# Optimization experiments

Measured on AMD Instinct MI355X. Metric: run time of the kernel, lower is better.

Reference implementation:

```python
import jax, jax.numpy as jnp
import numpy as np

IMAGE_SIZE = 288.0
LAMBDA_NOOBJ = 0.5
LAMBDA_COOR = 5.0
_ANCHOR_DIMS = np.array([[0.24, 0.24], [0.12, 0.12], [0.08, 0.08], [0.28, 0.28], [0.15, 0.15]], np.float32)
ANCHORS = jnp.concatenate([jnp.full((5, 2), 0.5, jnp.float32), jnp.asarray(_ANCHOR_DIMS)], axis=1)  # [cx,cy,w,h]


def _corners(box):
    # matches torch _format_bbox column order used in _get_iou: (x1, x2, y1, y2)
    cx, cy, w, h = box[..., 0], box[..., 1], box[..., 2], box[..., 3]
    return cx - w / 2, cx + w / 2, cy - h / 2, cy + h / 2


def _iou(b1, b2):
    x1a, x2a, y1a, y2a = _corners(b1)
    x1b, x2b, y1b, y2b = _corners(b2)
    iw = jnp.minimum(x2a, x2b) - jnp.maximum(x1a, x1b) + 1.0
    ih = jnp.minimum(y2a, y2b) - jnp.maximum(y1a, y1b) + 1.0
    inter = iw * ih
    a1 = (x2a - x1a + 1.0) * (y2a - y1a + 1.0)
    a2 = (x2b - x1b + 1.0) * (y2b - y1b + 1.0)
    return inter / (a1 + a2 - inter + 1e-16)


def setup_inputs() -> dict:
    key = jax.random.key(0)
    k1, k2, k3, k4 = jax.random.split(key, 4)
    B, G, A, T = 32, 36, 5, 8
    return {
        "bbox_prediction": jax.random.normal(k1, (B, G, G, A, 5), jnp.float32),
        "landmarks_prediction": jax.random.normal(k2, (B, G, G, A, 68, 2), jnp.float32),
        "bbox_target": jax.random.uniform(k3, (B, T, 4), jnp.float32),
        "landmarks_target": jax.random.uniform(k4, (B, T, 68, 2), jnp.float32),
    }


def _forward(bbox_prediction, landmarks_prediction, bbox_target, landmarks_target):
    B, G, _, A, _ = bbox_prediction.shape
    T = bbox_target.shape[1]
    N = B * G * G * A

    valid = bbox_target.sum(-1) != 0  # (B,T)
    gx = bbox_target[..., 0] * G
    gy = bbox_target[..., 1] * G
    gi = jnp.floor(gx).astype(jnp.int32)  # int(gt_x)
    gj = jnp.floor(gy).astype(jnp.int32)
    fx = gx - gi
    fy = gy - gj
    gt_anchor_box = jnp.stack([fx, fy, bbox_target[..., 2], bbox_target[..., 3]], -1)  # (B,T,4)

    # vectorized anchor assignment (replaces per-target python loop)
    anchor_iou = _iou(gt_anchor_box[:, :, None, :], ANCHORS[None, None, :, :])  # (B,T,A)
    best_a = jnp.argmax(anchor_iou, -1).astype(jnp.int32)
    log_box = jnp.log1p(gt_anchor_box)  # (B,T,4) -- torch stores log1p form

    lin = ((jnp.arange(B)[:, None] * G + gj) * G + gi) * A + best_a  # (B,T) flat (b,j,i,a)
    lin = jnp.where(valid, lin, N)  # invalid targets -> dump slot N

    obj = jnp.zeros(N + 1, jnp.float32).at[lin.ravel()].set(1.0)[:N].reshape(B, G, G, A)
    noobj = 1.0 - obj

    t_ids = jnp.broadcast_to(jnp.arange(T, dtype=jnp.int32), (B, T))
    seg_last = jax.ops.segment_max(t_ids.ravel(), lin.ravel(), num_segments=N + 1)
    winner = (seg_last[lin] == t_ids) & valid
    lin_w = jnp.where(winner, lin, N).ravel()

    gt_boxes = jnp.zeros((N + 1, 4), jnp.float32).at[lin_w].set(log_box.reshape(-1, 4))[:N].reshape(B, G, G, A, 4)
    gt_lm = jnp.zeros((N + 1, 136), jnp.float32).at[lin_w].set(landmarks_target.reshape(B * T, 136))[:N].reshape(B, G, G, A, 136)

    nobj = jnp.maximum(obj.sum(), 1.0)

    # NME over object cells (masked-mean expressed as weighted sum -> static shapes)
    diff = landmarks_prediction.reshape(B, G, G, A, 136) - gt_lm
    dist = jnp.sqrt(jnp.sum(diff * diff, -1))  # (B,G,G,A)
    wh = gt_boxes[..., 2] * gt_boxes[..., 3]  # note: log1p(w)*log1p(h), as in torch
    norm = jnp.sqrt(jnp.where(obj > 0, wh, 1.0)) * IMAGE_SIZE * 68.0 * nobj
    nme = jnp.sum(obj * dist / norm)

    # localization: SmoothL1 (beta=1), mean over masked elements
    d = bbox_prediction[..., :4] - gt_boxes
    ad = jnp.abs(d)
    sl1 = jnp.where(ad < 1.0, 0.5 * d * d, ad - 0.5)
    loc_loss = LAMBDA_COOR * jnp.sum(obj[..., None] * sl1) / (nobj * 4.0)

    # confidence: MSE on noobj (target 0) + MSE on obj (target 1)
    conf_pred = bbox_prediction[..., 4]
    n_noobj = jnp.maximum(noobj.sum(), 1.0)
    conf_loss = LAMBDA_NOOBJ * jnp.sum(noobj * conf_pred ** 2) / n_noobj + jnp.sum(obj * (conf_pred - 1.0) ** 2) / nobj

    # best predicted bbox per target (IoU of log1p gt box vs raw cell predictions, as in torch)
    cell_pred = bbox_prediction[jnp.arange(B)[:, None], gj, gi]  # (B,T,A,5)
    pred_iou = _iou(log_box[:, :, None, :], cell_pred[..., :4])  # (B,T,A)
    best_p = jnp.argmax(pred_iou, -1)
    best = jnp.take_along_axis(cell_pred, best_p[..., None, None], axis=2)[:, :, 0]  # (B,T,5)
    x1, x2, y1, y2 = _corners(best[..., :4])
    best_pred = jnp.where(valid[..., None], jnp.stack([x1, x2, y1, y2, best[..., 4]], -1), 0.0)

    return nme, loc_loss, conf_loss, best_pred


def reference(bbox_prediction, landmarks_prediction, bbox_target, landmarks_target):
    return _forward(bbox_prediction, landmarks_prediction, bbox_target, landmarks_target)
```

## Files before the change

### kernel.cpp

```cpp
#include <hip/hip_runtime.h>
#include <math.h>

#define Gc 36
#define Ac 5
#define Bc 32
#define Tc 8
#define NCELLS (Bc*Gc*Gc*Ac)
#define NFLOATS (NCELLS*5)
#define NF4 (NFLOATS/4)
#define NT 256
#define CONF_BLOCKS 128
#define GRID (CONF_BLOCKS + 256)


__device__ __forceinline__ void target_meta(const float* __restrict__ bbox_tgt,
                                            int tgt, bool& valid, int& gi, int& gj,
                                            float& fx, float& fy, float& w, float& h,
                                            int& best_a) {
    const float* tg = bbox_tgt + (size_t)tgt * 4;
    float x = tg[0], y = tg[1];
    w = tg[2]; h = tg[3];
    valid = ((x + y + w + h) != 0.0f);
    float gx = x * (float)Gc, gy = y * (float)Gc;
    gi = (int)floorf(gx); gj = (int)floorf(gy);
    fx = gx - floorf(gx); fy = gy - floorf(gy);

    float x1a = fx - w * 0.5f, x2a = fx + w * 0.5f;
    float y1a = fy - h * 0.5f, y2a = fy + h * 0.5f;
    float a1 = (x2a - x1a + 1.0f) * (y2a - y1a + 1.0f);
    const float adim[Ac] = {0.24f, 0.12f, 0.08f, 0.28f, 0.15f};
    best_a = 0;
    float best_iou = -1e30f;
    for (int a = 0; a < Ac; ++a) {
        float x1b = 0.5f - adim[a] * 0.5f, x2b = 0.5f + adim[a] * 0.5f;
        float iw = fminf(x2a, x2b) - fmaxf(x1a, x1b) + 1.0f;
        float ih = fminf(y2a, x2b) - fmaxf(y1a, x1b) + 1.0f;
        float inter = iw * ih;
        float a2 = (x2b - x1b + 1.0f) * (x2b - x1b + 1.0f);
        float iou = inter / (a1 + a2 - inter + 1e-16f);
        if (iou > best_iou) { best_iou = iou; best_a = a; }
    }
}

__device__ __forceinline__ void do_conf(const float* __restrict__ bbox_pred,
                                        float* __restrict__ ws_f) {
    __shared__ float red[NT];
    const float4* p4 = (const float4*)bbox_pred;
    float acc = 0.0f;
    for (int j = blockIdx.x * NT + threadIdx.x; j < NF4;
         j += CONF_BLOCKS * NT) {
        float4 f = p4[j];
        int r = (4 * j) % 5;
        float v = (r == 4) ? f.x : (r == 3) ? f.y : (r == 2) ? f.z
                : (r == 1) ? f.w : 0.0f;
        acc += v * v;
    }
    red[threadIdx.x] = acc;
    __syncthreads();
    for (int s = NT / 2; s > 0; s >>= 1) {
        if (threadIdx.x < s) red[threadIdx.x] += red[threadIdx.x + s];
        __syncthreads();
    }
    if (threadIdx.x == 0) ws_f[blockIdx.x] = red[0];
}

__device__ __forceinline__ void do_target(const float* __restrict__ lm_pred,
                                          const float* __restrict__ bbox_tgt,
                                          const float* __restrict__ lm_tgt,
                                          float* __restrict__ ws_f,
                                          int* __restrict__ ws_i) {
    const int tgt = blockIdx.x - CONF_BLOCKS;
    const int b = tgt >> 3, t = tgt & 7;
    const int tid = threadIdx.x;
    __shared__ int s_lin8[8];

    if (tid < 8) {
        bool v; int gi, gj, ba; float fx, fy, w, h;
        target_meta(bbox_tgt, (b << 3) + tid, v, gi, gj, fx, fy, w, h, ba);
        s_lin8[tid] = v ? (((b * Gc + gj) * Gc + gi) * Ac + ba) : NCELLS;
    }
    __syncthreads();

    if (tid < 64) {
        int lin = s_lin8[t];
        bool valid = (lin != NCELLS);
        bool winner = valid;
        if (valid)
            for (int t2 = t + 1; t2 < Tc; ++t2)
                if (s_lin8[t2] == lin) { winner = false; break; }

        float acc = 0.0f;
        if (winner && tid < 34) {
            const float4* lp = (const float4*)(lm_pred + (size_t)lin * 136);
            const float4* lt = (const float4*)(lm_tgt + (size_t)tgt * 136);
            float4 a = lp[tid], c = lt[tid];
            float dx = a.x - c.x, dy = a.y - c.y;
            float dz = a.z - c.z, dw = a.w - c.w;
            acc = dx * dx + dy * dy + dz * dz + dw * dw;
        }
        for (int off = 32; off > 0; off >>= 1)
            acc += __shfl_down(acc, off, 64);

        if (tid == 0) {
            ws_i[256 + tgt] = lin;
            ws_i[512 + tgt] = winner ? 1 : 0;
            ws_f[1024 + tgt] = winner ? sqrtf(acc) : 0.0f;
        }
    }
}

__device__ __forceinline__ void do_final(const float* __restrict__ bbox_pred,
                                         const float* __restrict__ bbox_tgt,
                                         const float* __restrict__ ws_f,
                                         const int* __restrict__ ws_i,
                                         float* __restrict__ out) {
    const int tid = threadIdx.x;
    const int b = tid >> 3;
    __shared__ float4 s_red4[NT];
    __shared__ float  s_reds[NT];
    __shared__ int    s_cnt[NT];

    bool valid; int gi, gj, best_a; float fx, fy, w, h;
    target_meta(bbox_tgt, tid, valid, gi, gj, fx, fy, w, h, best_a);
    int lin = ws_i[256 + tid];
    int winner = ws_i[512 + tid];
    float dist = ws_f[1024 + tid];

    float l0 = log1pf(fx), l1 = log1pf(fy), l2 = log1pf(w), l3 = log1pf(h);

    float c_nme = 0.0f, c_sl1 = 0.0f, c_cobj = 0.0f, c_csq = 0.0f;
    if (winner) {
        const float* bp = bbox_pred + (size_t)lin * 5;
        float conf = bp[4];
        c_cobj = (conf - 1.0f) * (conf - 1.0f);
        c_csq = conf * conf;
        float lb[4] = {l0, l1, l2, l3};
        for (int k = 0; k < 4; ++k) {
            float d = bp[k] - lb[k];
            float ad = fabsf(d);
            c_sl1 += (ad < 1.0f) ? 0.5f * d * d : (ad - 0.5f);
        }
        c_nme = dist / (sqrtf(l2 * l3) * 288.0f * 68.0f);
    }

    s_cnt[tid] = winner;
    s_red4[tid] = make_float4(c_nme, c_sl1, c_cobj, c_csq);
    s_reds[tid] = (tid < CONF_BLOCKS) ? ws_f[tid] : 0.0f;
    __syncthreads();
    for (int s = NT / 2; s > 0; s >>= 1) {
        if (tid < s) {
            s_cnt[tid] += s_cnt[tid + s];
            float4 a = s_red4[tid], c = s_red4[tid + s];
            a.x += c.x; a.y += c.y; a.z += c.z; a.w += c.w;
            s_red4[tid] = a;
            s_reds[tid] += s_reds[tid + s];
        }
        __syncthreads();
    }

    if (tid == 0) {
        int cnt = s_cnt[0];
        float nobj = fmaxf((float)cnt, 1.0f);
        float n_noobj = fmaxf((float)(NCELLS - cnt), 1.0f);
        float4 sums = s_red4[0];
        float s_total = s_reds[0];
        out[0] = sums.x / nobj;
        out[1] = 5.0f * sums.y / (nobj * 4.0f);
        out[2] = 0.5f * (s_total - sums.w) / n_noobj + sums.z / nobj;
    }

    const float* cp = bbox_pred + (size_t)((b * Gc + gj) * Gc + gi) * Ac * 5;
    float x1g = l0 - l2 * 0.5f, x2g = l0 + l2 * 0.5f;
    float y1g = l1 - l3 * 0.5f, y2g = l1 + l3 * 0.5f;
    float ag = (x2g - x1g + 1.0f) * (y2g - y1g + 1.0f);
    int bp_idx = 0;
    float bp_iou = -1e30f;
    for (int a = 0; a < Ac; ++a) {
        float cx = cp[a * 5 + 0], cy = cp[a * 5 + 1];
        float pw = cp[a * 5 + 2], ph = cp[a * 5 + 3];
        float x1p = cx - pw * 0.5f, x2p = cx + pw * 0.5f;
        float y1p = cy - ph * 0.5f, y2p = cy + ph * 0.5f;
        float iw = fminf(x2g, x2p) - fmaxf(x1g, x1p) + 1.0f;
        float ih = fminf(y2g, y2p) - fmaxf(y1g, y1p) + 1.0f;
        float inter = iw * ih;
        float ap = (x2p - x1p + 1.0f) * (y2p - y1p + 1.0f);
        float iou = inter / (ag + ap - inter + 1e-16f);
        if (iou > bp_iou) { bp_iou = iou; bp_idx = a; }
    }
    float bx = cp[bp_idx * 5 + 0], by = cp[bp_idx * 5 + 1];
    float bw = cp[bp_idx * 5 + 2], bh = cp[bp_idx * 5 + 3];
    float bconf = cp[bp_idx * 5 + 4];
    float* op = out + 3 + (size_t)tid * 5;
    if (valid) {
        op[0] = bx - bw * 0.5f; op[1] = bx + bw * 0.5f;
        op[2] = by - bh * 0.5f; op[3] = by + bh * 0.5f; op[4] = bconf;
    } else {
        op[0] = 0.0f; op[1] = 0.0f; op[2] = 0.0f; op[3] = 0.0f; op[4] = 0.0f;
    }
}

__global__ __launch_bounds__(NT) void k_all(
        const float* __restrict__ bbox_pred,
        const float* __restrict__ lm_pred,
        const float* __restrict__ bbox_tgt,
        const float* __restrict__ lm_tgt,
        float* ws_f, int* ws_i,
        float* __restrict__ out) {
    if (blockIdx.x < CONF_BLOCKS) {
        do_conf(bbox_pred, ws_f);
    } else {
        do_target(lm_pred, bbox_tgt, lm_tgt, ws_f, ws_i);
    }

    __shared__ int s_last;
    if (threadIdx.x == 0) {
        __threadfence();
        unsigned int old = atomicAdd((unsigned int*)(ws_i + 2048), 1u);
        int last = (old == (unsigned int)(GRID - 1));
        if (last) __threadfence();
        s_last = last;
    }
    __syncthreads();

    if (s_last) {
        do_final(bbox_pred, bbox_tgt, ws_f, ws_i, out);
    }
}

extern "C" void kernel_launch(void* const* d_in, const int* in_sizes, int n_in,
                              void* d_out, int out_size, void* d_ws, size_t ws_size,
                              hipStream_t stream) {
    const float* bbox_pred = (const float*)d_in[0];
    const float* lm_pred   = (const float*)d_in[1];
    const float* bbox_tgt  = (const float*)d_in[2];
    const float* lm_tgt    = (const float*)d_in[3];
    float* out = (float*)d_out;
    float* ws_f = (float*)d_ws;
    int* ws_i = (int*)d_ws;

    hipMemsetAsync((char*)d_ws + 2048 * sizeof(int), 0, sizeof(unsigned int),
                   stream);

    k_all<<<GRID, NT, 0, stream>>>(bbox_pred, lm_pred, bbox_tgt, lm_tgt,
                                   ws_f, ws_i, out);
}
```

Measured before the change: 162.9 us.

## Replace last-block atomic handoff with two kernel launches and move best-pred to target blocks

Splits the single fused kernel, which used an atomic counter with threadfences to pick the last block for the final reduction, into two launches: one for the confidence and landmark partials and one single-block final kernel. This drops the memset and the atomic/fence handshake. The best-predicted-box IoU search moves from the final block into the per-target blocks, so the final kernel's serial tail is shorter. In exchange there is an extra kernel launch boundary.

New measurement: 152.4 us. 6.4% less time.

```diff
diff --git a/kernel.cpp b/kernel.cpp
--- a/kernel.cpp
+++ b/kernel.cpp
@@ -10,7 +10,6 @@
 #define NF4 (NFLOATS/4)
 #define NT 256
 #define CONF_BLOCKS 128
-#define GRID (CONF_BLOCKS + 256)
 
 
 __device__ __forceinline__ void target_meta(const float* __restrict__ bbox_tgt,
@@ -42,80 +41,119 @@
     }
 }
 
-__device__ __forceinline__ void do_conf(const float* __restrict__ bbox_pred,
-                                        float* __restrict__ ws_f) {
-    __shared__ float red[NT];
-    const float4* p4 = (const float4*)bbox_pred;
-    float acc = 0.0f;
-    for (int j = blockIdx.x * NT + threadIdx.x; j < NF4;
-         j += CONF_BLOCKS * NT) {
-        float4 f = p4[j];
-        int r = (4 * j) % 5;
-        float v = (r == 4) ? f.x : (r == 3) ? f.y : (r == 2) ? f.z
-                : (r == 1) ? f.w : 0.0f;
-        acc += v * v;
-    }
-    red[threadIdx.x] = acc;
-    __syncthreads();
-    for (int s = NT / 2; s > 0; s >>= 1) {
-        if (threadIdx.x < s) red[threadIdx.x] += red[threadIdx.x + s];
+__global__ __launch_bounds__(NT) void k12_conf_lm(
+        const float* __restrict__ bbox_pred,
+        const float* __restrict__ lm_pred,
+        const float* __restrict__ bbox_tgt,
+        const float* __restrict__ lm_tgt,
+        float* __restrict__ ws_f, int* __restrict__ ws_i,
+        float* __restrict__ out) {
+    if (blockIdx.x < CONF_BLOCKS) {
+        __shared__ float red[NT];
+        const float4* p4 = (const float4*)bbox_pred;
+        float acc = 0.0f;
+        for (int j = blockIdx.x * NT + threadIdx.x; j < NF4;
+             j += CONF_BLOCKS * NT) {
+            float4 f = p4[j];
+            int r = (4 * j) % 5;
+            float v = (r == 4) ? f.x : (r == 3) ? f.y : (r == 2) ? f.z
+                    : (r == 1) ? f.w : 0.0f;
+            acc += v * v;
+        }
+        red[threadIdx.x] = acc;
         __syncthreads();
-    }
-    if (threadIdx.x == 0) ws_f[blockIdx.x] = red[0];
-}
-
-__device__ __forceinline__ void do_target(const float* __restrict__ lm_pred,
-                                          const float* __restrict__ bbox_tgt,
-                                          const float* __restrict__ lm_tgt,
-                                          float* __restrict__ ws_f,
-                                          int* __restrict__ ws_i) {
-    const int tgt = blockIdx.x - CONF_BLOCKS;
-    const int b = tgt >> 3, t = tgt & 7;
+        for (int s = NT / 2; s > 0; s >>= 1) {
+            if (threadIdx.x < s) red[threadIdx.x] += red[threadIdx.x + s];
+            __syncthreads();
+        }
+        if (threadIdx.x == 0) ws_f[blockIdx.x] = red[0];
+    } else {
+        const int tgt = blockIdx.x - CONF_BLOCKS;
+        const int b = tgt >> 3, t = tgt & 7;
+        const int tid = threadIdx.x;
+        __shared__ int s_lin8[8];
+
+        if (tid < 8) {
+            bool v; int gi, gj, ba; float fx, fy, w, h;
+            target_meta(bbox_tgt, (b << 3) + tid, v, gi, gj, fx, fy, w, h, ba);
+            s_lin8[tid] = v ? (((b * Gc + gj) * Gc + gi) * Ac + ba) : NCELLS;
+        }
+        __syncthreads();
+
+        if (tid < 64) {
+            int lin = s_lin8[t];
+            bool valid = (lin != NCELLS);
+            bool winner = valid;
+            if (valid)
+                for (int t2 = t + 1; t2 < Tc; ++t2)
+                    if (s_lin8[t2] == lin) { winner = false; break; }
+
+            float acc = 0.0f;
+            if (winner && tid < 34) {
+                const float4* lp = (const float4*)(lm_pred + (size_t)lin * 136);
+                const float4* lt = (const float4*)(lm_tgt + (size_t)tgt * 136);
+                float4 a = lp[tid], c = lt[tid];
+                float dx = a.x - c.x, dy = a.y - c.y;
+                float dz = a.z - c.z, dw = a.w - c.w;
+                acc = dx * dx + dy * dy + dz * dz + dw * dw;
+            }
+            for (int off = 32; off > 0; off >>= 1)
+                acc += __shfl_down(acc, off, 64);
+
+            if (tid == 0) {
+                ws_i[256 + tgt] = lin;
+                ws_i[512 + tgt] = winner ? 1 : 0;
+                ws_f[1024 + tgt] = winner ? sqrtf(acc) : 0.0f;
+            }
+        }
+
+        if (tid == 0) {
+            bool valid; int gi, gj, best_a; float fx, fy, w, h;
+            target_meta(bbox_tgt, tgt, valid, gi, gj, fx, fy, w, h, best_a);
+            float l0 = log1pf(fx), l1 = log1pf(fy);
+            float l2 = log1pf(w),  l3 = log1pf(h);
+
+            const float* cp = bbox_pred
+                            + (size_t)((b * Gc + gj) * Gc + gi) * Ac * 5;
+            float x1g = l0 - l2 * 0.5f, x2g = l0 + l2 * 0.5f;
+            float y1g = l1 - l3 * 0.5f, y2g = l1 + l3 * 0.5f;
+            float ag = (x2g - x1g + 1.0f) * (y2g - y1g + 1.0f);
+            int bp_idx = 0;
+            float bp_iou = -1e30f;
+            for (int a = 0; a < Ac; ++a) {
+                float cx = cp[a * 5 + 0], cy = cp[a * 5 + 1];
+                float pw = cp[a * 5 + 2], ph = cp[a * 5 + 3];
+                float x1p = cx - pw * 0.5f, x2p = cx + pw * 0.5f;
+                float y1p = cy - ph * 0.5f, y2p = cy + ph * 0.5f;
+                float iw = fminf(x2g, x2p) - fmaxf(x1g, x1p) + 1.0f;
+                float ih = fminf(y2g, y2p) - fmaxf(y1g, y1p) + 1.0f;
+                float inter = iw * ih;
+                float ap = (x2p - x1p + 1.0f) * (y2p - y1p + 1.0f);
+                float iou = inter / (ag + ap - inter + 1e-16f);
+                if (iou > bp_iou) { bp_iou = iou; bp_idx = a; }
+            }
+            float bx = cp[bp_idx * 5 + 0], by = cp[bp_idx * 5 + 1];
+            float bw = cp[bp_idx * 5 + 2], bh = cp[bp_idx * 5 + 3];
+            float bconf = cp[bp_idx * 5 + 4];
+            float* op = out + 3 + (size_t)tgt * 5;
+            if (valid) {
+                op[0] = bx - bw * 0.5f; op[1] = bx + bw * 0.5f;
+                op[2] = by - bh * 0.5f; op[3] = by + bh * 0.5f; op[4] = bconf;
+            } else {
+                op[0] = 0.0f; op[1] = 0.0f; op[2] = 0.0f;
+                op[3] = 0.0f; op[4] = 0.0f;
+            }
+        }
+    }
+}
+
+__global__ __launch_bounds__(NT) void k3_final(
+        const float* __restrict__ bbox_pred,
+        const float* __restrict__ bbox_tgt,
+        const float* __restrict__ ws_f,
+        const int* __restrict__ ws_i,
+        float* __restrict__ out) {
     const int tid = threadIdx.x;
-    __shared__ int s_lin8[8];
-
-    if (tid < 8) {
-        bool v; int gi, gj, ba; float fx, fy, w, h;
-        target_meta(bbox_tgt, (b << 3) + tid, v, gi, gj, fx, fy, w, h, ba);
-        s_lin8[tid] = v ? (((b * Gc + gj) * Gc + gi) * Ac + ba) : NCELLS;
-    }
-    __syncthreads();
-
-    if (tid < 64) {
-        int lin = s_lin8[t];
-        bool valid = (lin != NCELLS);
-        bool winner = valid;
-        if (valid)
-            for (int t2 = t + 1; t2 < Tc; ++t2)
-                if (s_lin8[t2] == lin) { winner = false; break; }
-
-        float acc = 0.0f;
-        if (winner && tid < 34) {
-            const float4* lp = (const float4*)(lm_pred + (size_t)lin * 136);
-            const float4* lt = (const float4*)(lm_tgt + (size_t)tgt * 136);
-            float4 a = lp[tid], c = lt[tid];
-            float dx = a.x - c.x, dy = a.y - c.y;
-            float dz = a.z - c.z, dw = a.w - c.w;
-            acc = dx * dx + dy * dy + dz * dz + dw * dw;
-        }
-        for (int off = 32; off > 0; off >>= 1)
-            acc += __shfl_down(acc, off, 64);
-
-        if (tid == 0) {
-            ws_i[256 + tgt] = lin;
-            ws_i[512 + tgt] = winner ? 1 : 0;
-            ws_f[1024 + tgt] = winner ? sqrtf(acc) : 0.0f;
-        }
-    }
-}
-
-__device__ __forceinline__ void do_final(const float* __restrict__ bbox_pred,
-                                         const float* __restrict__ bbox_tgt,
-                                         const float* __restrict__ ws_f,
-                                         const int* __restrict__ ws_i,
-                                         float* __restrict__ out) {
-    const int tid = threadIdx.x;
-    const int b = tid >> 3;
     __shared__ float4 s_red4[NT];
     __shared__ float  s_reds[NT];
     __shared__ int    s_cnt[NT];
@@ -168,63 +206,6 @@
         out[1] = 5.0f * sums.y / (nobj * 4.0f);
         out[2] = 0.5f * (s_total - sums.w) / n_noobj + sums.z / nobj;
     }
-
-    const float* cp = bbox_pred + (size_t)((b * Gc + gj) * Gc + gi) * Ac * 5;
-    float x1g = l0 - l2 * 0.5f, x2g = l0 + l2 * 0.5f;
-    float y1g = l1 - l3 * 0.5f, y2g = l1 + l3 * 0.5f;
-    float ag = (x2g - x1g + 1.0f) * (y2g - y1g + 1.0f);
-    int bp_idx = 0;
-    float bp_iou = -1e30f;
-    for (int a = 0; a < Ac; ++a) {
-        float cx = cp[a * 5 + 0], cy = cp[a * 5 + 1];
-        float pw = cp[a * 5 + 2], ph = cp[a * 5 + 3];
-        float x1p = cx - pw * 0.5f, x2p = cx + pw * 0.5f;
-        float y1p = cy - ph * 0.5f, y2p = cy + ph * 0.5f;
-        float iw = fminf(x2g, x2p) - fmaxf(x1g, x1p) + 1.0f;
-        float ih = fminf(y2g, y2p) - fmaxf(y1g, y1p) + 1.0f;
-        float inter = iw * ih;
-        float ap = (x2p - x1p + 1.0f) * (y2p - y1p + 1.0f);
-        float iou = inter / (ag + ap - inter + 1e-16f);
-        if (iou > bp_iou) { bp_iou = iou; bp_idx = a; }
-    }
-    float bx = cp[bp_idx * 5 + 0], by = cp[bp_idx * 5 + 1];
-    float bw = cp[bp_idx * 5 + 2], bh = cp[bp_idx * 5 + 3];
-    float bconf = cp[bp_idx * 5 + 4];
-    float* op = out + 3 + (size_t)tid * 5;
-    if (valid) {
-        op[0] = bx - bw * 0.5f; op[1] = bx + bw * 0.5f;
-        op[2] = by - bh * 0.5f; op[3] = by + bh * 0.5f; op[4] = bconf;
-    } else {
-        op[0] = 0.0f; op[1] = 0.0f; op[2] = 0.0f; op[3] = 0.0f; op[4] = 0.0f;
-    }
-}
-
-__global__ __launch_bounds__(NT) void k_all(
-        const float* __restrict__ bbox_pred,
-        const float* __restrict__ lm_pred,
-        const float* __restrict__ bbox_tgt,
-        const float* __restrict__ lm_tgt,
-        float* ws_f, int* ws_i,
-        float* __restrict__ out) {
-    if (blockIdx.x < CONF_BLOCKS) {
-        do_conf(bbox_pred, ws_f);
-    } else {
-        do_target(lm_pred, bbox_tgt, lm_tgt, ws_f, ws_i);
-    }
-
-    __shared__ int s_last;
-    if (threadIdx.x == 0) {
-        __threadfence();
-        unsigned int old = atomicAdd((unsigned int*)(ws_i + 2048), 1u);
-        int last = (old == (unsigned int)(GRID - 1));
-        if (last) __threadfence();
-        s_last = last;
-    }
-    __syncthreads();
-
-    if (s_last) {
-        do_final(bbox_pred, bbox_tgt, ws_f, ws_i, out);
-    }
 }
 
 extern "C" void kernel_launch(void* const* d_in, const int* in_sizes, int n_in,
@@ -238,9 +219,8 @@
     float* ws_f = (float*)d_ws;
     int* ws_i = (int*)d_ws;
 
-    hipMemsetAsync((char*)d_ws + 2048 * sizeof(int), 0, sizeof(unsigned int),
-                   stream);
-
-    k_all<<<GRID, NT, 0, stream>>>(bbox_pred, lm_pred, bbox_tgt, lm_tgt,
-                                   ws_f, ws_i, out);
-}
+    k12_conf_lm<<<CONF_BLOCKS + 256, NT, 0, stream>>>(bbox_pred, lm_pred,
+                                                      bbox_tgt, lm_tgt,
+                                                      ws_f, ws_i, out);
+    k3_final<<<1, NT, 0, stream>>>(bbox_pred, bbox_tgt, ws_f, ws_i, out);
+}
```
